# Performance work log

Measured on AMD Instinct MI355X. Metric: run time of the kernel, lower is better.

The kernel has to match this reference:

```python
import jax, jax.numpy as jnp
import numpy as np
import math

H = 16
D_MODEL = 1024
B, S = 2, 2048

def setup_inputs() -> dict:
    key = jax.random.key(0)
    ks = jax.random.split(key, 7)
    q = jax.random.normal(ks[0], (B, S, D_MODEL), dtype=jnp.float32)
    k = jax.random.normal(ks[1], (B, S, D_MODEL), dtype=jnp.float32)
    v = jax.random.normal(ks[2], (B, S, D_MODEL), dtype=jnp.float32)
    mask = jnp.ones((1, 1, S, S), dtype=jnp.int32)
    sc = 1.0 / math.sqrt(D_MODEL)
    W_Q = jax.random.normal(ks[3], (D_MODEL, D_MODEL), dtype=jnp.float32) * sc
    W_K = jax.random.normal(ks[4], (D_MODEL, D_MODEL), dtype=jnp.float32) * sc
    W_V = jax.random.normal(ks[5], (D_MODEL, D_MODEL), dtype=jnp.float32) * sc
    W_T = jax.random.normal(ks[6], (D_MODEL, D_MODEL), dtype=jnp.float32) * sc
    return {"q": q, "k": k, "v": v, "mask": mask, "W_Q": W_Q, "W_K": W_K, "W_V": W_V, "W_T": W_T}

def reference(q, k, v, mask, W_Q, W_K, W_V, W_T):
    # W matrices stored as (in, out); nn.Linear applies x @ W.T with W (out,in),
    # equivalent here since we treat these directly as projection matrices.
    def split_heads(x):  # [B,S,D] -> [B,H,S,hd]
        Bq, Sq, Dq = x.shape
        return x.reshape(Bq, Sq, H, Dq // H).transpose(0, 2, 1, 3)

    Q = split_heads(q @ W_Q)
    K = split_heads(k @ W_K)
    V = split_heads(v @ W_V)
    d_k = Q.shape[-1]
    score = jnp.einsum("bhqd,bhkd->bhqk", Q, K) / math.sqrt(d_k)
    score = jnp.where(mask == 0, jnp.float32(-1e9), score)
    attn = jax.nn.softmax(score, axis=-1)
    out = jnp.einsum("bhqk,bhkd->bhqd", attn, V)
    out = out.transpose(0, 2, 1, 3).reshape(q.shape[0], q.shape[1], D_MODEL)
    return out @ W_T
```

## Files before the change

kernel.cpp:

```cpp
#include <hip/hip_runtime.h>
#include <hip/hip_bf16.h>
#include <stdint.h>

#define H  16
#define DM 1024
#define BB 2
#define SS 2048
#define HD 64

#define QSCALE 0.18033688011112042f
#define MASKVAL -57.7078f

typedef __attribute__((ext_vector_type(8))) short bf16x8;
typedef __attribute__((ext_vector_type(4))) float f32x4;

__device__ __forceinline__ short f2bf(float f) {
  __hip_bfloat16 h = __float2bfloat16(f);
  return *reinterpret_cast<short*>(&h);
}

__device__ __forceinline__ unsigned pack_bf16(float a, float b) {
#if __has_builtin(__builtin_amdgcn_cvt_pk_bf16_f32)
  typedef __attribute__((ext_vector_type(2))) __bf16 bf16x2_t;
  bf16x2_t p = __builtin_amdgcn_cvt_pk_bf16_f32(a, b);
  unsigned u;
  __builtin_memcpy(&u, &p, 4);
  return u;
#else
  unsigned ua = __builtin_bit_cast(unsigned, a);
  unsigned ub = __builtin_bit_cast(unsigned, b);
  ua = (ua + 0x7FFFu + ((ua >> 16) & 1u)) >> 16;
  ub = (ub + 0x7FFFu + ((ub >> 16) & 1u));
  return (ub & 0xFFFF0000u) | ua;
#endif
}

__device__ __forceinline__ void load16_lds(const short* g, short* l) {
  __builtin_amdgcn_global_load_lds(
      (const __attribute__((address_space(1))) void*)g,
      (__attribute__((address_space(3))) void*)l, 16, 0, 0);
}

__global__ void prep_kernel(const float* __restrict__ Wq, const float* __restrict__ Wk,
                            const float* __restrict__ Wv, const float* __restrict__ Wt,
                            short* __restrict__ WTall,
                            const float* __restrict__ q, const float* __restrict__ k,
                            const float* __restrict__ v, short* __restrict__ Abf,
                            const int4* __restrict__ mask4, int* __restrict__ flag) {
  int z = blockIdx.z;
  int t = threadIdx.x;
  if (z < 4) {
    if (blockIdx.x >= 1024) return;
    __shared__ short tile[32][33];
    const float* src = (z == 0) ? Wq : (z == 1) ? Wk : (z == 2) ? Wv : Wt;
    short* out = WTall + (size_t)z * DM * DM;
    int c0 = (blockIdx.x & 31) * 32, r0 = (blockIdx.x >> 5) * 32;
    int tx = t & 31, ty = t >> 5;
    for (int j = 0; j < 4; j++)
      tile[ty + j * 8][tx] = f2bf(src[(size_t)(r0 + ty + j * 8) * DM + c0 + tx]);
    __syncthreads();
    for (int j = 0; j < 4; j++)
      out[(size_t)(c0 + ty + j * 8) * DM + r0 + tx] = tile[tx][ty + j * 8];
  } else if (z < 7) {
    int zz = z - 4;
    const float* src = (zz == 0) ? q : (zz == 1) ? k : v;
    short* out = Abf + (size_t)zz * BB * SS * DM;
    size_t i = ((size_t)blockIdx.x * 256 + t) * 4;
    float4 f = *(const float4*)&src[i];
    uint2 p = {pack_bf16(f.x, f.y), pack_bf16(f.z, f.w)};
    *(uint2*)&out[i] = p;
  } else {
    int idx = blockIdx.x * 256 + t;
    int4 m = mask4[idx];
    if (m.x == 0 || m.y == 0 || m.z == 0 || m.w == 0) atomicOr(flag, 1);
  }
}

__global__ void transpose_w_kernel(const float* __restrict__ Wq, const float* __restrict__ Wk,
                                   const float* __restrict__ Wv, const float* __restrict__ Wt,
                                   short* __restrict__ dst, int* __restrict__ flag) {
  if (blockIdx.x == 0 && blockIdx.y == 0 && blockIdx.z == 0 &&
      threadIdx.y == 0 && threadIdx.x < 2) flag[threadIdx.x] = 0;
  __shared__ short tile[32][33];
  int z = blockIdx.z;
  const float* src = (z == 0) ? Wq : (z == 1) ? Wk : (z == 2) ? Wv : Wt;
  short* out = dst + (size_t)z * DM * DM;
  int c0 = blockIdx.x * 32, r0 = blockIdx.y * 32;
  int tx = threadIdx.x, ty = threadIdx.y;
  for (int j = 0; j < 4; j++)
    tile[ty + j * 8][tx] = f2bf(src[(size_t)(r0 + ty + j * 8) * DM + c0 + tx]);
  __syncthreads();
  for (int j = 0; j < 4; j++)
    out[(size_t)(c0 + ty + j * 8) * DM + r0 + tx] = tile[tx][ty + j * 8];
}

__global__ void mask_scan_kernel(const int4* __restrict__ mask4, int n4, int* __restrict__ flag) {
  int idx = blockIdx.x * blockDim.x + threadIdx.x;
  int stride = gridDim.x * blockDim.x;
  int any = 0;
  for (int i = idx; i < n4; i += stride) {
    int4 m = mask4[i];
    if (m.x == 0 || m.y == 0 || m.z == 0 || m.w == 0) any = 1;
  }
  if (any) atomicOr(flag, 1);
}

__global__ void flag_init_kernel(int* flag) { if (threadIdx.x < 2) flag[threadIdx.x] = 0; }

__global__ void transpose_v_kernel(const short* __restrict__ Vbuf, short* __restrict__ Vt) {
  __shared__ short tile[32][33];
  int bh = blockIdx.z;
  int s0 = blockIdx.x * 32, d0 = blockIdx.y * 32;
  int tx = threadIdx.x, ty = threadIdx.y;
  for (int j = 0; j < 4; j++)
    tile[ty + j * 8][tx] = Vbuf[((size_t)bh * SS + s0 + ty + j * 8) * HD + d0 + tx];
  __syncthreads();
  for (int j = 0; j < 4; j++)
    Vt[((size_t)bh * HD + d0 + ty + j * 8) * SS + s0 + tx] = tile[tx][ty + j * 8];
}

__global__ void signal_fill_kernel(float* __restrict__ out, int n) {
  int i = blockIdx.x * blockDim.x + threadIdx.x;
  if (i < n) out[i] = 1.0f;
}

template <int AF32>
__device__ __forceinline__ void gemm_fast_body(const void* __restrict__ Av,
                                               const short* __restrict__ Bt,
                                               void* __restrict__ Cv, int mode, float scale) {
  __shared__ __align__(16) short As[128 * 32];
  __shared__ __align__(16) short Bs[128 * 32];
  int m0 = blockIdx.x * 128, n0 = blockIdx.y * 128;
  int t = threadIdx.x;
  int lane = t & 63, w = t >> 6;
  int l16 = lane & 15, quad = lane >> 4;
  int wm = (w >> 1) * 64, wn = (w & 1) * 64;
  f32x4 acc[4][4] = {};

  for (int k0 = 0; k0 < DM; k0 += 32) {
    if (AF32) {
      const float* A = (const float*)Av;
      for (int i = 0; i < 4; i++) {
        int c = t + i * 256;
        int row = c >> 3, seg = c & 7;
        float4 f = *(const float4*)&A[(size_t)(m0 + row) * DM + k0 + seg * 4];
        uint2 p = {pack_bf16(f.x, f.y), pack_bf16(f.z, f.w)};
        *(uint2*)&As[row * 32 + seg * 4] = p;
      }
    } else {
      const short* A = (const short*)Av;
      for (int i = 0; i < 2; i++) {
        int c = t + i * 256;
        load16_lds(&A[(size_t)(m0 + (c >> 2)) * DM + k0 + (c & 3) * 8], &As[c * 8]);
      }
    }
    for (int i = 0; i < 2; i++) {
      int c = t + i * 256;
      load16_lds(&Bt[(size_t)(n0 + (c >> 2)) * DM + k0 + (c & 3) * 8], &Bs[c * 8]);
    }
    __syncthreads();
    bf16x8 af[4], bfr[4];
    for (int i = 0; i < 4; i++) af[i]  = *(const bf16x8*)&As[(wm + i * 16 + l16) * 32 + quad * 8];
    for (int i = 0; i < 4; i++) bfr[i] = *(const bf16x8*)&Bs[(wn + i * 16 + l16) * 32 + quad * 8];
    for (int mi = 0; mi < 4; mi++)
      for (int ni = 0; ni < 4; ni++)
        acc[mi][ni] = __builtin_amdgcn_mfma_f32_16x16x32_bf16(af[mi], bfr[ni], acc[mi][ni], 0, 0, 0);
    __syncthreads();
  }

  for (int mi = 0; mi < 4; mi++)
    for (int ni = 0; ni < 4; ni++)
      for (int r = 0; r < 4; r++) {
        int m = m0 + wm + mi * 16 + quad * 4 + r;
        int n = n0 + wn + ni * 16 + l16;
        if (mode == 0) {
          short* C = (short*)Cv;
          int b = m >> 11, s = m & (SS - 1);
          int h = n >> 6, d = n & (HD - 1);
          C[(((size_t)(b * H + h) * SS) + s) * HD + d] = f2bf(acc[mi][ni][r] * scale);
        } else {
          float* C = (float*)Cv;
          C[(size_t)m * DM + n] = acc[mi][ni][r];
        }
      }
}

template <int AF32>
__global__ __launch_bounds__(256, 3) void gemm_qkv_fast_kernel(
    const void* __restrict__ A0, const void* __restrict__ A1, const void* __restrict__ A2,
    const short* __restrict__ WTall,
    short* __restrict__ Qb, short* __restrict__ Kb, short* __restrict__ Vb) {
  int z = blockIdx.z;
  const void* A = (z == 0) ? A0 : (z == 1) ? A1 : A2;
  const short* B = WTall + (size_t)z * DM * DM;
  short* C = (z == 0) ? Qb : (z == 1) ? Kb : Vb;
  gemm_fast_body<AF32>(A, B, (void*)C, 0, (z == 0) ? QSCALE : 1.0f);
}

__global__ __launch_bounds__(256, 3) void gemm_out_fast_kernel(
    const short* __restrict__ Obuf, const short* __restrict__ WtT, float* __restrict__ out) {
  gemm_fast_body<0>((const void*)Obuf, WtT, (void*)out, 2, 1.0f);
}

#define LDT 40
#define LDB 136

template <int AF32>
__device__ __forceinline__ void gemm_legacy_body(const void* __restrict__ Av,
                                                 const float* __restrict__ Bm,
                                                 void* __restrict__ Cv, int mode, float scale) {
  __shared__ __align__(16) short As[128 * LDT];
  __shared__ __align__(16) short Bsh[32 * LDB];
  int m0 = blockIdx.x * 128, n0 = blockIdx.y * 128;
  int t = threadIdx.x;
  int lane = t & 63, w = t >> 6;
  int l16 = lane & 15, quad = lane >> 4;
  int wm = (w >> 1) * 64, wn = (w & 1) * 64;
  f32x4 acc[4][4] = {};

  for (int k0 = 0; k0 < DM; k0 += 32) {
    if (AF32) {
      const float* A = (const float*)Av;
      for (int i = 0; i < 4; i++) {
        int c = t + i * 256;
        int row = c >> 3, seg = c & 7;
        float4 f = *(const float4*)&A[(size_t)(m0 + row) * DM + k0 + seg * 4];
        uint2 p = {pack_bf16(f.x, f.y), pack_bf16(f.z, f.w)};
        *(uint2*)&As[row * LDT + seg * 4] = p;
      }
    } else {
      const short* A = (const short*)Av;
      for (int i = 0; i < 2; i++) {
        int c = t + i * 256;
        int row = c >> 2, seg = c & 3;
        *(int4*)&As[row * LDT + seg * 8] = *(const int4*)&A[(size_t)(m0 + row) * DM + k0 + seg * 8];
      }
    }
    for (int i = 0; i < 4; i++) {
      int c = t + i * 256;
      int krow = c >> 5, nseg = c & 31;
      float4 f = *(const float4*)&Bm[(size_t)(k0 + krow) * DM + n0 + nseg * 4];
      uint2 p = {pack_bf16(f.x, f.y), pack_bf16(f.z, f.w)};
      *(uint2*)&Bsh[krow * LDB + nseg * 4] = p;
    }
    __syncthreads();
    bf16x8 af[4], bfr[4];
    for (int i = 0; i < 4; i++) af[i] = *(const bf16x8*)&As[(wm + i * 16 + l16) * LDT + quad * 8];
    for (int i = 0; i < 4; i++) {
      bf16x8 tmp;
      for (int j = 0; j < 8; j++) tmp[j] = Bsh[(quad * 8 + j) * LDB + wn + i * 16 + l16];
      bfr[i] = tmp;
    }
    for (int mi = 0; mi < 4; mi++)
      for (int ni = 0; ni < 4; ni++)
        acc[mi][ni] = __builtin_amdgcn_mfma_f32_16x16x32_bf16(af[mi], bfr[ni], acc[mi][ni], 0, 0, 0);
    __syncthreads();
  }

  for (int mi = 0; mi < 4; mi++)
    for (int ni = 0; ni < 4; ni++)
      for (int r = 0; r < 4; r++) {
        int m = m0 + wm + mi * 16 + quad * 4 + r;
        int n = n0 + wn + ni * 16 + l16;
        if (mode == 0) {
          short* C = (short*)Cv;
          int b = m >> 11, s = m & (SS - 1);
          int h = n >> 6, d = n & (HD - 1);
          C[(((size_t)(b * H + h) * SS) + s) * HD + d] = f2bf(acc[mi][ni][r] * scale);
        } else {
          float* C = (float*)Cv;
          C[(size_t)m * DM + n] = acc[mi][ni][r];
        }
      }
}

__global__ __launch_bounds__(256, 2) void gemm_qkv_legacy_kernel(
    const float* __restrict__ q, const float* __restrict__ k, const float* __restrict__ v,
    const float* __restrict__ B0, const float* __restrict__ B1, const float* __restrict__ B2,
    short* __restrict__ Qb, short* __restrict__ Kb, short* __restrict__ Vb) {
  int z = blockIdx.z;
  const float* A = (z == 0) ? q : (z == 1) ? k : v;
  const float* B = (z == 0) ? B0 : (z == 1) ? B1 : B2;
  short* C = (z == 0) ? Qb : (z == 1) ? Kb : Vb;
  gemm_legacy_body<1>((const void*)A, B, (void*)C, 0, (z == 0) ? QSCALE : 1.0f);
}

__global__ __launch_bounds__(256, 2) void gemm_out_legacy_kernel(
    const short* __restrict__ Obuf, const float* __restrict__ Wt, float* __restrict__ out) {
  gemm_legacy_body<0>((const void*)Obuf, Wt, (void*)out, 2, 1.0f);
}

#define LDP 72

template <int UM>
__device__ __forceinline__ void attn_tile(
    const short* __restrict__ Ksb, const short* __restrict__ Vsb,
    short* __restrict__ Psw, const bf16x8 aq[2], f32x4 oacc[4], float& lsum,
    const int* __restrict__ mask, int qg, int kb) {
  int lane = threadIdx.x & 63;
  int l16 = lane & 15, quad = lane >> 4;

#pragma unroll
  for (int kb2 = 0; kb2 < 4; kb2++) {
    int krow = kb2 * 16 + l16;
    bf16x8 k0 = *(const bf16x8*)&Ksb[krow * 64 + ((quad ^ (l16 & 7)) * 8)];
    bf16x8 k1 = *(const bf16x8*)&Ksb[krow * 64 + (((quad + 4) ^ (l16 & 7)) * 8)];
    f32x4 sc = {};
    sc = __builtin_amdgcn_mfma_f32_16x16x32_bf16(k0, aq[0], sc, 0, 0, 0);
    sc = __builtin_amdgcn_mfma_f32_16x16x32_bf16(k1, aq[1], sc, 0, 0, 0);
    if (UM) {
#pragma unroll
      for (int r = 0; r < 4; r++) {
        int kg = kb + kb2 * 16 + quad * 4 + r;
        if (mask[(size_t)qg * SS + kg] == 0) sc[r] = MASKVAL;
      }
    }
    float p0 = __builtin_exp2f(sc[0]);
    float p1 = __builtin_exp2f(sc[1]);
    float p2 = __builtin_exp2f(sc[2]);
    float p3 = __builtin_exp2f(sc[3]);
    lsum += (p0 + p1) + (p2 + p3);
    uint2 packed = {pack_bf16(p0, p1), pack_bf16(p2, p3)};
    *(uint2*)&Psw[l16 * LDP + kb2 * 16 + quad * 4] = packed;
  }

  __builtin_amdgcn_s_setprio(1);
#pragma unroll
  for (int c = 0; c < 2; c++) {
    bf16x8 ap = *(const bf16x8*)&Psw[l16 * LDP + c * 32 + quad * 8];
#pragma unroll
    for (int nb2 = 0; nb2 < 4; nb2++) {
      bf16x8 bv = *(const bf16x8*)&Vsb[(nb2 * 16 + l16) * 64 + (((c * 4 + quad) ^ (l16 & 7)) * 8)];
      oacc[nb2] = __builtin_amdgcn_mfma_f32_16x16x32_bf16(ap, bv, oacc[nb2], 0, 0, 0);
    }
  }
  __builtin_amdgcn_s_setprio(0);
}

__global__ __launch_bounds__(512, 4) void attn128_kernel(
    const short* __restrict__ Q, const short* __restrict__ K,
    const short* __restrict__ Vt, const int* __restrict__ mask,
    const int* __restrict__ flag, short* __restrict__ O) {
  __shared__ __align__(16) short Ks[2][64 * 64];
  __shared__ __align__(16) short Vs[2][64 * 64];
  __shared__ __align__(16) short Ps[8][16 * LDP];

  int bx = blockIdx.x, by = blockIdx.y;
  int bh = (bx & 7) * 4 + (by >> 3);
  int qt = (by & 7) * 2 + (bx >> 3);
  int q0 = qt * 128;

  int t = threadIdx.x, lane = t & 63, w = t >> 6;
  int l16 = lane & 15, quad = lane >> 4;
  int use_mask = flag[0];

  const short* qrow = Q + ((size_t)bh * SS + q0 + w * 16 + l16) * HD;
  bf16x8 aq[2] = {*(const bf16x8*)&qrow[quad * 8], *(const bf16x8*)&qrow[32 + quad * 8]};

  float lsum = 0.f;
  f32x4 oacc[4] = {};

  const short* Kbase = K  + (size_t)bh * SS * HD;
  const short* Vbase = Vt + (size_t)bh * HD * SS;

  int rp = t >> 3, lc = (t & 7) ^ (rp & 7);
  const short* kSrc = &Kbase[(size_t)rp * HD + lc * 8];
  const short* vSrc = &Vbase[(size_t)rp * SS + lc * 8];
  int qg = q0 + w * 16 + l16;

  load16_lds(kSrc, &Ks[0][t * 8]);
  load16_lds(vSrc, &Vs[0][t * 8]);
  asm volatile("s_waitcnt vmcnt(0)" ::: "memory");
  __builtin_amdgcn_s_barrier();

  int cur = 0;
  if (!use_mask) {
    for (int kt = 0; kt < SS / 64 - 1; kt++) {
      int kb1 = (kt + 1) * 64;
      load16_lds(kSrc + (size_t)kb1 * HD, &Ks[cur ^ 1][t * 8]);
      load16_lds(vSrc + kb1, &Vs[cur ^ 1][t * 8]);
      attn_tile<0>(Ks[cur], Vs[cur], Ps[w], aq, oacc, lsum, mask, qg, kt * 64);
      asm volatile("s_waitcnt vmcnt(0)" ::: "memory");
      __builtin_amdgcn_s_barrier();
      cur ^= 1;
    }
    attn_tile<0>(Ks[cur], Vs[cur], Ps[w], aq, oacc, lsum, mask, qg, SS - 64);
  } else {
    for (int kt = 0; kt < SS / 64 - 1; kt++) {
      int kb1 = (kt + 1) * 64;
      load16_lds(kSrc + (size_t)kb1 * HD, &Ks[cur ^ 1][t * 8]);
      load16_lds(vSrc + kb1, &Vs[cur ^ 1][t * 8]);
      attn_tile<1>(Ks[cur], Vs[cur], Ps[w], aq, oacc, lsum, mask, qg, kt * 64);
      asm volatile("s_waitcnt vmcnt(0)" ::: "memory");
      __builtin_amdgcn_s_barrier();
      cur ^= 1;
    }
    attn_tile<1>(Ks[cur], Vs[cur], Ps[w], aq, oacc, lsum, mask, qg, SS - 64);
  }

  lsum += __shfl_xor(lsum, 16);
  lsum += __shfl_xor(lsum, 32);

  int b = bh >> 4, h = bh & 15;
#pragma unroll
  for (int r = 0; r < 4; r++) {
    float inv = 1.0f / __shfl(lsum, quad * 4 + r);
    int qq = q0 + w * 16 + quad * 4 + r;
#pragma unroll
    for (int nb2 = 0; nb2 < 4; nb2++) {
      int d = nb2 * 16 + l16;
      O[((size_t)(b * SS + qq)) * DM + h * HD + d] = f2bf(oacc[nb2][r] * inv);
    }
  }
}

__global__ __launch_bounds__(256, 4) void attn64_kernel(
    const short* __restrict__ Q, const short* __restrict__ K,
    const short* __restrict__ V, const int* __restrict__ mask,
    const int* __restrict__ flag, short* __restrict__ O) {
  __shared__ __align__(16) short Ks[64 * 64];
  __shared__ __align__(16) short Vs[64 * 64];
  __shared__ __align__(16) short Ps[4][16 * LDP];

  int bh = blockIdx.y;
  int q0 = blockIdx.x * 64;
  int t = threadIdx.x, lane = t & 63, w = t >> 6;
  int l16 = lane & 15, quad = lane >> 4;
  int use_mask = flag[0];

  const short* qrow = Q + ((size_t)bh * SS + q0 + w * 16 + l16) * HD;
  bf16x8 aq0 = *(const bf16x8*)&qrow[quad * 8];
  bf16x8 aq1 = *(const bf16x8*)&qrow[32 + quad * 8];

  float lsum[4] = {0.f, 0.f, 0.f, 0.f};
  f32x4 oacc[4] = {};

  const short* Kbase = K + (size_t)bh * SS * HD;
  const short* Vbase = V + (size_t)bh * SS * HD;
  int dd = t & 63, h2 = t >> 6;

  for (int kt = 0; kt < SS / 64; kt++) {
    int kb = kt * 64;
    for (int i = 0; i < 2; i++) {
      int p = t + i * 256;
      int rp = p >> 3, cp = p & 7;
      int lc = cp ^ (rp & 7);
      load16_lds(&Kbase[(size_t)(kb + rp) * HD + lc * 8], &Ks[p * 8]);
    }
    for (int sgi = 0; sgi < 2; sgi++) {
      int sg = h2 * 2 + sgi;
      short tmp[8];
      for (int jj = 0; jj < 8; jj++)
        tmp[jj] = Vbase[(size_t)(kb + sg * 8 + jj) * HD + dd];
      *(int4*)&Vs[dd * 64 + ((sg ^ (dd & 7)) * 8)] = *(const int4*)tmp;
    }
    __syncthreads();

    for (int nb = 0; nb < 4; nb++) {
      f32x4 sc = {};
      bf16x8 bk0 = *(const bf16x8*)&Ks[(nb * 16 + l16) * 64 + ((quad ^ (l16 & 7)) * 8)];
      bf16x8 bk1 = *(const bf16x8*)&Ks[(nb * 16 + l16) * 64 + (((quad + 4) ^ (l16 & 7)) * 8)];
      sc = __builtin_amdgcn_mfma_f32_16x16x32_bf16(aq0, bk0, sc, 0, 0, 0);
      sc = __builtin_amdgcn_mfma_f32_16x16x32_bf16(aq1, bk1, sc, 0, 0, 0);
      if (use_mask) {
        int kg = kb + nb * 16 + l16;
        for (int r = 0; r < 4; r++) {
          int qg = q0 + w * 16 + quad * 4 + r;
          if (mask[(size_t)qg * SS + kg] == 0) sc[r] = MASKVAL;
        }
      }
      for (int r = 0; r < 4; r++) {
        float pv = __builtin_exp2f(sc[r]);
        lsum[r] += pv;
        Ps[w][(quad * 4 + r) * LDP + nb * 16 + l16] = f2bf(pv);
      }
    }

    for (int c = 0; c < 2; c++) {
      bf16x8 ap = *(const bf16x8*)&Ps[w][l16 * LDP + c * 32 + quad * 8];
      for (int nb2 = 0; nb2 < 4; nb2++) {
        bf16x8 bv = *(const bf16x8*)&Vs[(nb2 * 16 + l16) * 64 + (((c * 4 + quad) ^ (l16 & 7)) * 8)];
        oacc[nb2] = __builtin_amdgcn_mfma_f32_16x16x32_bf16(ap, bv, oacc[nb2], 0, 0, 0);
      }
    }
    __syncthreads();
  }

  for (int st = 1; st < 16; st <<= 1)
    for (int r = 0; r < 4; r++) lsum[r] += __shfl_xor(lsum[r], st);

  int b = bh >> 4, h = bh & 15;
  for (int r = 0; r < 4; r++) {
    float inv = 1.0f / lsum[r];
    int qg = q0 + w * 16 + quad * 4 + r;
    for (int nb2 = 0; nb2 < 4; nb2++) {
      int d = nb2 * 16 + l16;
      O[((size_t)(b * SS + qg)) * DM + h * HD + d] = f2bf(oacc[nb2][r] * inv);
    }
  }
}

extern "C" void kernel_launch(void* const* d_in, const int* in_sizes, int n_in,
                              void* d_out, int out_size, void* d_ws, size_t ws_size,
                              hipStream_t stream) {
  const float* q    = (const float*)d_in[0];
  const float* k    = (const float*)d_in[1];
  const float* v    = (const float*)d_in[2];
  const int*   mask = (const int*)d_in[3];
  const float* Wq   = (const float*)d_in[4];
  const float* Wk   = (const float*)d_in[5];
  const float* Wv   = (const float*)d_in[6];
  const float* Wt   = (const float*)d_in[7];
  float* out = (float*)d_out;

  char* ws = (char*)d_ws;
  const size_t MB = 1024ull * 1024ull;
  const size_t NEED_A = 66 * MB;
  const size_t NEED_B = 40 * MB + 4096;
  const size_t NEED_C = 32 * MB + 4096;

  if (ws_size >= NEED_A) {
    short* WTall = (short*)(ws);
    short* Qbuf  = (short*)(ws + 8 * MB);
    short* Kbuf  = (short*)(ws + 16 * MB);
    short* Vbuf  = (short*)(ws + 24 * MB);
    short* Obuf  = (short*)(ws + 32 * MB);
    int*   flag  = (int*)(ws + 40 * MB);
    short* Abf   = (short*)(ws + 41 * MB);
    short* Vt    = Abf;

    hipMemsetAsync(flag, 0, 8, stream);
    prep_kernel<<<dim3(4096, 1, 8), 256, 0, stream>>>(
        Wq, Wk, Wv, Wt, WTall, q, k, v, Abf, (const int4*)mask, flag);
    gemm_qkv_fast_kernel<0><<<dim3(BB * SS / 128, DM / 128, 3), 256, 0, stream>>>(
        Abf, Abf + (size_t)BB * SS * DM, Abf + 2ull * BB * SS * DM, WTall, Qbuf, Kbuf, Vbuf);
    transpose_v_kernel<<<dim3(SS / 32, HD / 32, BB * H), dim3(32, 8), 0, stream>>>(Vbuf, Vt);
    attn128_kernel<<<dim3(SS / 128, BB * H), 512, 0, stream>>>(Qbuf, Kbuf, Vt, mask, flag, Obuf);
    gemm_out_fast_kernel<<<dim3(BB * SS / 128, DM / 128), 256, 0, stream>>>(
        Obuf, WTall + 3ull * DM * DM, out);
  } else if (ws_size >= NEED_B) {
    short* WTall = (short*)(ws);
    short* Qbuf  = (short*)(ws + 8 * MB);
    short* Kbuf  = (short*)(ws + 16 * MB);
    short* Vbuf  = (short*)(ws + 24 * MB);
    short* Obuf  = (short*)(ws + 32 * MB);
    int*   flag  = (int*)(ws + 40 * MB);

    transpose_w_kernel<<<dim3(32, 32, 4), dim3(32, 8), 0, stream>>>(Wq, Wk, Wv, Wt, WTall, flag);
    mask_scan_kernel<<<512, 256, 0, stream>>>((const int4*)mask, SS * SS / 4, flag);
    gemm_qkv_fast_kernel<1><<<dim3(BB * SS / 128, DM / 128, 3), 256, 0, stream>>>(
        q, k, v, WTall, Qbuf, Kbuf, Vbuf);
    attn64_kernel<<<dim3(SS / 64, BB * H), 256, 0, stream>>>(Qbuf, Kbuf, Vbuf, mask, flag, Obuf);
    gemm_out_fast_kernel<<<dim3(BB * SS / 128, DM / 128), 256, 0, stream>>>(
        Obuf, WTall + 3ull * DM * DM, out);
  } else if (ws_size >= NEED_C) {
    short* Qbuf = (short*)(ws);
    short* Kbuf = (short*)(ws + 8 * MB);
    short* Vbuf = (short*)(ws + 16 * MB);
    short* Obuf = (short*)(ws + 24 * MB);
    int*   flag = (int*)(ws + 32 * MB);

    flag_init_kernel<<<1, 64, 0, stream>>>(flag);
    mask_scan_kernel<<<512, 256, 0, stream>>>((const int4*)mask, SS * SS / 4, flag);
    gemm_qkv_legacy_kernel<<<dim3(BB * SS / 128, DM / 128, 3), 256, 0, stream>>>(
        q, k, v, Wq, Wk, Wv, Qbuf, Kbuf, Vbuf);
    attn64_kernel<<<dim3(SS / 64, BB * H), 256, 0, stream>>>(Qbuf, Kbuf, Vbuf, mask, flag, Obuf);
    gemm_out_legacy_kernel<<<dim3(BB * SS / 128, DM / 128), 256, 0, stream>>>(Obuf, Wt, out);
  } else {
    signal_fill_kernel<<<(BB * SS * DM + 255) / 256, 256, 0, stream>>>(out, BB * SS * DM);
  }
}
```

Measured before the change: 253.5 us.

## Deepen GEMM K-tile with XOR-swizzled LDS and emit transposed V from projection

The fast GEMM body now stages a 64-wide K tile per iteration instead of 32, halving the number of barrier pairs, and uses an XOR swizzle on LDS rows to avoid bank conflicts on the fragment reads. The V projection is computed as W_V^T times v so the GEMM writes V already transposed per head, which removes the separate transpose_v kernel and its extra pass over V. LDS use doubles, so launch bounds drop from 3 to 2 blocks per SM, and the transposed-output epilogue writes with a different store pattern that may coalesce less well.

```diff
diff --git a/kernel.cpp b/kernel.cpp
--- a/kernel.cpp
+++ b/kernel.cpp
@@ -107,18 +107,6 @@
 
 __global__ void flag_init_kernel(int* flag) { if (threadIdx.x < 2) flag[threadIdx.x] = 0; }
 
-__global__ void transpose_v_kernel(const short* __restrict__ Vbuf, short* __restrict__ Vt) {
-  __shared__ short tile[32][33];
-  int bh = blockIdx.z;
-  int s0 = blockIdx.x * 32, d0 = blockIdx.y * 32;
-  int tx = threadIdx.x, ty = threadIdx.y;
-  for (int j = 0; j < 4; j++)
-    tile[ty + j * 8][tx] = Vbuf[((size_t)bh * SS + s0 + ty + j * 8) * HD + d0 + tx];
-  __syncthreads();
-  for (int j = 0; j < 4; j++)
-    Vt[((size_t)bh * HD + d0 + ty + j * 8) * SS + s0 + tx] = tile[tx][ty + j * 8];
-}
-
 __global__ void signal_fill_kernel(float* __restrict__ out, int n) {
   int i = blockIdx.x * blockDim.x + threadIdx.x;
   if (i < n) out[i] = 1.0f;
@@ -127,9 +115,119 @@
 template <int AF32>
 __device__ __forceinline__ void gemm_fast_body(const void* __restrict__ Av,
                                                const short* __restrict__ Bt,
-                                               void* __restrict__ Cv, int mode, float scale) {
-  __shared__ __align__(16) short As[128 * 32];
-  __shared__ __align__(16) short Bs[128 * 32];
+                                               void* __restrict__ Cv, int mode, float scale,
+                                               int m0, int n0) {
+  __shared__ __align__(16) short As[128 * 64];
+  __shared__ __align__(16) short Bs[128 * 64];
+  int t = threadIdx.x;
+  int lane = t & 63, w = t >> 6;
+  int l16 = lane & 15, quad = lane >> 4;
+  int wm = (w >> 1) * 64, wn = (w & 1) * 64;
+  f32x4 acc[4][4] = {};
+
+  for (int k0 = 0; k0 < DM; k0 += 64) {
+    if (AF32) {
+      const float* A = (const float*)Av;
+#pragma unroll
+      for (int i = 0; i < 8; i++) {
+        int c = t + i * 256;
+        int row = c >> 4, hseg = c & 15;
+        int lseg = (hseg >> 1) ^ (row & 7);
+        float4 f = *(const float4*)&A[(size_t)(m0 + row) * DM + k0 + hseg * 4];
+        uint2 p = {pack_bf16(f.x, f.y), pack_bf16(f.z, f.w)};
+        *(uint2*)&As[row * 64 + lseg * 8 + (hseg & 1) * 4] = p;
+      }
+    } else {
+      const short* A = (const short*)Av;
+#pragma unroll
+      for (int i = 0; i < 4; i++) {
+        int c = t + i * 256;
+        int row = c >> 3, seg = c & 7;
+        int lseg = seg ^ (row & 7);
+        load16_lds(&A[(size_t)(m0 + row) * DM + k0 + lseg * 8], &As[c * 8]);
+      }
+    }
+#pragma unroll
+    for (int i = 0; i < 4; i++) {
+      int c = t + i * 256;
+      int row = c >> 3, seg = c & 7;
+      int lseg = seg ^ (row & 7);
+      load16_lds(&Bt[(size_t)(n0 + row) * DM + k0 + lseg * 8], &Bs[c * 8]);
+    }
+    __syncthreads();
+#pragma unroll
+    for (int h = 0; h < 2; h++) {
+      bf16x8 af[4], bfr[4];
+#pragma unroll
+      for (int i = 0; i < 4; i++)
+        af[i] = *(const bf16x8*)&As[(wm + i * 16 + l16) * 64 + (((h * 4 + quad) ^ (l16 & 7)) * 8)];
+#pragma unroll
+      for (int i = 0; i < 4; i++)
+        bfr[i] = *(const bf16x8*)&Bs[(wn + i * 16 + l16) * 64 + (((h * 4 + quad) ^ (l16 & 7)) * 8)];
+#pragma unroll
+      for (int mi = 0; mi < 4; mi++)
+#pragma unroll
+        for (int ni = 0; ni < 4; ni++)
+          acc[mi][ni] = __builtin_amdgcn_mfma_f32_16x16x32_bf16(af[mi], bfr[ni], acc[mi][ni], 0, 0, 0);
+    }
+    __syncthreads();
+  }
+
+  for (int mi = 0; mi < 4; mi++)
+    for (int ni = 0; ni < 4; ni++)
+      for (int r = 0; r < 4; r++) {
+        int m = m0 + wm + mi * 16 + quad * 4 + r;
+        int n = n0 + wn + ni * 16 + l16;
+        if (mode == 0) {
+          short* C = (short*)Cv;
+          int b = m >> 11, s = m & (SS - 1);
+          int h = n >> 6, d = n & (HD - 1);
+          C[(((size_t)(b * H + h) * SS) + s) * HD + d] = f2bf(acc[mi][ni][r] * scale);
+        } else if (mode == 3) {
+          short* C = (short*)Cv;
+          int h = m >> 6, d = m & (HD - 1);
+          int b = n >> 11, s = n & (SS - 1);
+          C[((size_t)(b * H + h) * HD + d) * SS + s] = f2bf(acc[mi][ni][r] * scale);
+        } else {
+          float* C = (float*)Cv;
+          C[(size_t)m * DM + n] = acc[mi][ni][r];
+        }
+      }
+}
+
+template <int AF32, int VT>
+__global__ __launch_bounds__(256, 2) void gemm_qkv_fast_kernel(
+    const void* __restrict__ A0, const void* __restrict__ A1, const void* __restrict__ A2,
+    const short* __restrict__ WTall,
+    short* __restrict__ Qb, short* __restrict__ Kb, short* __restrict__ Vb) {
+  int z = blockIdx.z;
+  if (VT && z == 2) {
+    gemm_fast_body<0>((const void*)(WTall + 2ull * DM * DM), (const short*)A2, (void*)Vb,
+                      3, 1.0f, blockIdx.y * 128, blockIdx.x * 128);
+  } else {
+    const void* A = (z == 0) ? A0 : (z == 1) ? A1 : A2;
+    const short* B = WTall + (size_t)z * DM * DM;
+    short* C = (z == 0) ? Qb : (z == 1) ? Kb : Vb;
+    gemm_fast_body<AF32>(A, B, (void*)C, 0, (z == 0) ? QSCALE : 1.0f,
+                         blockIdx.x * 128, blockIdx.y * 128);
+  }
+}
+
+__global__ __launch_bounds__(256, 2) void gemm_out_fast_kernel(
+    const short* __restrict__ Obuf, const short* __restrict__ WtT, float* __restrict__ out) {
+  gemm_fast_body<0>((const void*)Obuf, WtT, (void*)out, 2, 1.0f,
+                    blockIdx.x * 128, blockIdx.y * 128);
+}
+
+#define LDT 40
+#define LDB 136
+
+template <int AF32>
+__device__ __forceinline__ void gemm_legacy_body(const void* __restrict__ Av,
+                                                 const float* __restrict__ Bm,
+                                                 void* __restrict__ Cv, int mode, float scale) {
+  __shared__ __align__(16) short As[128 * LDT];
+  __shared__ __align__(16) short Bsh[32 * LDB];
   int m0 = blockIdx.x * 128, n0 = blockIdx.y * 128;
   int t = threadIdx.x;
   int lane = t & 63, w = t >> 6;
@@ -145,23 +243,31 @@
         int row = c >> 3, seg = c & 7;
         float4 f = *(const float4*)&A[(size_t)(m0 + row) * DM + k0 + seg * 4];
         uint2 p = {pack_bf16(f.x, f.y), pack_bf16(f.z, f.w)};
-        *(uint2*)&As[row * 32 + seg * 4] = p;
+        *(uint2*)&As[row * LDT + seg * 4] = p;
       }
     } else {
       const short* A = (const short*)Av;
       for (int i = 0; i < 2; i++) {
         int c = t + i * 256;
-        load16_lds(&A[(size_t)(m0 + (c >> 2)) * DM + k0 + (c & 3) * 8], &As[c * 8]);
-      }
-    }
-    for (int i = 0; i < 2; i++) {
+        int row = c >> 2, seg = c & 3;
+        *(int4*)&As[row * LDT + seg * 8] = *(const int4*)&A[(size_t)(m0 + row) * DM + k0 + seg * 8];
+      }
+    }
+    for (int i = 0; i < 4; i++) {
       int c = t + i * 256;
-      load16_lds(&Bt[(size_t)(n0 + (c >> 2)) * DM + k0 + (c & 3) * 8], &Bs[c * 8]);
+      int krow = c >> 5, nseg = c & 31;
+      float4 f = *(const float4*)&Bm[(size_t)(k0 + krow) * DM + n0 + nseg * 4];
+      uint2 p = {pack_bf16(f.x, f.y), pack_bf16(f.z, f.w)};
+      *(uint2*)&Bsh[krow * LDB + nseg * 4] = p;
     }
     __syncthreads();
     bf16x8 af[4], bfr[4];
-    for (int i = 0; i < 4; i++) af[i]  = *(const bf16x8*)&As[(wm + i * 16 + l16) * 32 + quad * 8];
-    for (int i = 0; i < 4; i++) bfr[i] = *(const bf16x8*)&Bs[(wn + i * 16 + l16) * 32 + quad * 8];
+    for (int i = 0; i < 4; i++) af[i] = *(const bf16x8*)&As[(wm + i * 16 + l16) * LDT + quad * 8];
+    for (int i = 0; i < 4; i++) {
+      bf16x8 tmp;
+      for (int j = 0; j < 8; j++) tmp[j] = Bsh[(quad * 8 + j) * LDB + wn + i * 16 + l16];
+      bfr[i] = tmp;
+    }
     for (int mi = 0; mi < 4; mi++)
       for (int ni = 0; ni < 4; ni++)
         acc[mi][ni] = __builtin_amdgcn_mfma_f32_16x16x32_bf16(af[mi], bfr[ni], acc[mi][ni], 0, 0, 0);
@@ -185,95 +291,6 @@
       }
 }
 
-template <int AF32>
-__global__ __launch_bounds__(256, 3) void gemm_qkv_fast_kernel(
-    const void* __restrict__ A0, const void* __restrict__ A1, const void* __restrict__ A2,
-    const short* __restrict__ WTall,
-    short* __restrict__ Qb, short* __restrict__ Kb, short* __restrict__ Vb) {
-  int z = blockIdx.z;
-  const void* A = (z == 0) ? A0 : (z == 1) ? A1 : A2;
-  const short* B = WTall + (size_t)z * DM * DM;
-  short* C = (z == 0) ? Qb : (z == 1) ? Kb : Vb;
-  gemm_fast_body<AF32>(A, B, (void*)C, 0, (z == 0) ? QSCALE : 1.0f);
-}
-
-__global__ __launch_bounds__(256, 3) void gemm_out_fast_kernel(
-    const short* __restrict__ Obuf, const short* __restrict__ WtT, float* __restrict__ out) {
-  gemm_fast_body<0>((const void*)Obuf, WtT, (void*)out, 2, 1.0f);
-}
-
-#define LDT 40
-#define LDB 136
-
-template <int AF32>
-__device__ __forceinline__ void gemm_legacy_body(const void* __restrict__ Av,
-                                                 const float* __restrict__ Bm,
-                                                 void* __restrict__ Cv, int mode, float scale) {
-  __shared__ __align__(16) short As[128 * LDT];
-  __shared__ __align__(16) short Bsh[32 * LDB];
-  int m0 = blockIdx.x * 128, n0 = blockIdx.y * 128;
-  int t = threadIdx.x;
-  int lane = t & 63, w = t >> 6;
-  int l16 = lane & 15, quad = lane >> 4;
-  int wm = (w >> 1) * 64, wn = (w & 1) * 64;
-  f32x4 acc[4][4] = {};
-
-  for (int k0 = 0; k0 < DM; k0 += 32) {
-    if (AF32) {
-      const float* A = (const float*)Av;
-      for (int i = 0; i < 4; i++) {
-        int c = t + i * 256;
-        int row = c >> 3, seg = c & 7;
-        float4 f = *(const float4*)&A[(size_t)(m0 + row) * DM + k0 + seg * 4];
-        uint2 p = {pack_bf16(f.x, f.y), pack_bf16(f.z, f.w)};
-        *(uint2*)&As[row * LDT + seg * 4] = p;
-      }
-    } else {
-      const short* A = (const short*)Av;
-      for (int i = 0; i < 2; i++) {
-        int c = t + i * 256;
-        int row = c >> 2, seg = c & 3;
-        *(int4*)&As[row * LDT + seg * 8] = *(const int4*)&A[(size_t)(m0 + row) * DM + k0 + seg * 8];
-      }
-    }
-    for (int i = 0; i < 4; i++) {
-      int c = t + i * 256;
-      int krow = c >> 5, nseg = c & 31;
-      float4 f = *(const float4*)&Bm[(size_t)(k0 + krow) * DM + n0 + nseg * 4];
-      uint2 p = {pack_bf16(f.x, f.y), pack_bf16(f.z, f.w)};
-      *(uint2*)&Bsh[krow * LDB + nseg * 4] = p;
-    }
-    __syncthreads();
-    bf16x8 af[4], bfr[4];
-    for (int i = 0; i < 4; i++) af[i] = *(const bf16x8*)&As[(wm + i * 16 + l16) * LDT + quad * 8];
-    for (int i = 0; i < 4; i++) {
-      bf16x8 tmp;
-      for (int j = 0; j < 8; j++) tmp[j] = Bsh[(quad * 8 + j) * LDB + wn + i * 16 + l16];
-      bfr[i] = tmp;
-    }
-    for (int mi = 0; mi < 4; mi++)
-      for (int ni = 0; ni < 4; ni++)
-        acc[mi][ni] = __builtin_amdgcn_mfma_f32_16x16x32_bf16(af[mi], bfr[ni], acc[mi][ni], 0, 0, 0);
-    __syncthreads();
-  }
-
-  for (int mi = 0; mi < 4; mi++)
-    for (int ni = 0; ni < 4; ni++)
-      for (int r = 0; r < 4; r++) {
-        int m = m0 + wm + mi * 16 + quad * 4 + r;
-        int n = n0 + wn + ni * 16 + l16;
-        if (mode == 0) {
-          short* C = (short*)Cv;
-          int b = m >> 11, s = m & (SS - 1);
-          int h = n >> 6, d = n & (HD - 1);
-          C[(((size_t)(b * H + h) * SS) + s) * HD + d] = f2bf(acc[mi][ni][r] * scale);
-        } else {
-          float* C = (float*)Cv;
-          C[(size_t)m * DM + n] = acc[mi][ni][r];
-        }
-      }
-}
-
 __global__ __launch_bounds__(256, 2) void gemm_qkv_legacy_kernel(
     const float* __restrict__ q, const float* __restrict__ k, const float* __restrict__ v,
     const float* __restrict__ B0, const float* __restrict__ B1, const float* __restrict__ B2,
@@ -523,19 +540,17 @@
     short* WTall = (short*)(ws);
     short* Qbuf  = (short*)(ws + 8 * MB);
     short* Kbuf  = (short*)(ws + 16 * MB);
-    short* Vbuf  = (short*)(ws + 24 * MB);
+    short* Vtbuf = (short*)(ws + 24 * MB);
     short* Obuf  = (short*)(ws + 32 * MB);
     int*   flag  = (int*)(ws + 40 * MB);
     short* Abf   = (short*)(ws + 41 * MB);
-    short* Vt    = Abf;
 
     hipMemsetAsync(flag, 0, 8, stream);
     prep_kernel<<<dim3(4096, 1, 8), 256, 0, stream>>>(
         Wq, Wk, Wv, Wt, WTall, q, k, v, Abf, (const int4*)mask, flag);
-    gemm_qkv_fast_kernel<0><<<dim3(BB * SS / 128, DM / 128, 3), 256, 0, stream>>>(
-        Abf, Abf + (size_t)BB * SS * DM, Abf + 2ull * BB * SS * DM, WTall, Qbuf, Kbuf, Vbuf);
-    transpose_v_kernel<<<dim3(SS / 32, HD / 32, BB * H), dim3(32, 8), 0, stream>>>(Vbuf, Vt);
-    attn128_kernel<<<dim3(SS / 128, BB * H), 512, 0, stream>>>(Qbuf, Kbuf, Vt, mask, flag, Obuf);
+    gemm_qkv_fast_kernel<0, 1><<<dim3(BB * SS / 128, DM / 128, 3), 256, 0, stream>>>(
+        Abf, Abf + (size_t)BB * SS * DM, Abf + 2ull * BB * SS * DM, WTall, Qbuf, Kbuf, Vtbuf);
+    attn128_kernel<<<dim3(SS / 128, BB * H), 512, 0, stream>>>(Qbuf, Kbuf, Vtbuf, mask, flag, Obuf);
     gemm_out_fast_kernel<<<dim3(BB * SS / 128, DM / 128), 256, 0, stream>>>(
         Obuf, WTall + 3ull * DM * DM, out);
   } else if (ws_size >= NEED_B) {
@@ -548,7 +563,7 @@
 
     transpose_w_kernel<<<dim3(32, 32, 4), dim3(32, 8), 0, stream>>>(Wq, Wk, Wv, Wt, WTall, flag);
     mask_scan_kernel<<<512, 256, 0, stream>>>((const int4*)mask, SS * SS / 4, flag);
-    gemm_qkv_fast_kernel<1><<<dim3(BB * SS / 128, DM / 128, 3), 256, 0, stream>>>(
+    gemm_qkv_fast_kernel<1, 0><<<dim3(BB * SS / 128, DM / 128, 3), 256, 0, stream>>>(
         q, k, v, WTall, Qbuf, Kbuf, Vbuf);
     attn64_kernel<<<dim3(SS / 64, BB * H), 256, 0, stream>>>(Qbuf, Kbuf, Vbuf, mask, flag, Obuf);
     gemm_out_fast_kernel<<<dim3(BB * SS / 128, DM / 128), 256, 0, stream>>>(
```

After: 237.0 us. -6.5%, faster.
